# Kernel optimization log

Measured on AMD Instinct MI355X. Metric: run time of the kernel, lower is better.

Reference implementation:

```python
import jax, jax.numpy as jnp
import numpy as np
from jax import lax


def _c1x1(t, w, b=None):
    # t: [B,C,H,W], w: [O,C] (1x1 conv == channel matmul)
    y = jnp.einsum('bchw,oc->bohw', t, w)
    if b is not None:
        y = y + b[None, :, None, None]
    return y


def _mamba(u, in_w, conv_w, conv_b, xproj_w, dt_w, dt_b, A_log, Dp, out_w):
    # u: [B,L,d_model]; Mamba block (mamba_ssm defaults: in/out/x_proj bias=False)
    B, L, _ = u.shape
    d_inner = conv_w.shape[0]
    d_state = A_log.shape[1]
    dt_rank = dt_w.shape[1]
    d_conv = conv_w.shape[2]
    xz = jnp.einsum('bld,ed->ble', u, in_w)          # [B,L,2*d_inner]
    xc, z = xz[..., :d_inner], xz[..., d_inner:]
    # depthwise causal conv1d over seq
    xt = jnp.pad(xc.transpose(0, 2, 1), ((0, 0), (0, 0), (d_conv - 1, 0)))
    xt = lax.conv_general_dilated(xt, conv_w, (1,), 'VALID',
                                  feature_group_count=d_inner,
                                  dimension_numbers=('NCH', 'OIH', 'NCH'))
    xc = jax.nn.silu(xt + conv_b[None, :, None]).transpose(0, 2, 1)  # [B,L,d_inner]
    dbc = jnp.einsum('bld,ed->ble', xc, xproj_w)     # [B,L,dt_rank+2*d_state]
    dt = dbc[..., :dt_rank]
    B_ = dbc[..., dt_rank:dt_rank + d_state]
    C_ = dbc[..., dt_rank + d_state:]
    delta = jax.nn.softplus(jnp.einsum('blr,dr->bld', dt, dt_w) + dt_b)  # [B,L,d_inner]
    A = -jnp.exp(A_log)                              # [d_inner,d_state]
    dA = jnp.exp(delta[..., None] * A)               # [B,L,D,N]
    dBu = delta[..., None] * B_[:, :, None, :] * xc[..., None]
    def step(h, inp):
        dA_t, dBu_t, c_t = inp
        h = dA_t * h + dBu_t                         # [B,D,N]
        y = jnp.einsum('bdn,bn->bd', h, c_t)
        return h, y
    h0 = jnp.zeros((B, d_inner, d_state), dtype=u.dtype)
    _, ys = lax.scan(step, h0, (dA.transpose(1, 0, 2, 3),
                                dBu.transpose(1, 0, 2, 3),
                                C_.transpose(1, 0, 2)))
    y = ys.transpose(1, 0, 2) + xc * Dp              # [B,L,d_inner]
    y = y * jax.nn.silu(z)
    return jnp.einsum('bld,od->blo', y, out_w)       # [B,L,d_model]


def setup_inputs() -> dict:
    key = jax.random.key(0)
    B, C, H, W = 8, 128, 160, 160
    mip, d_in, d_st, d_r, d_cv = 8, 256, 16, 8, 4
    ks = iter(jax.random.split(key, 64))
    def rn(shape, s=0.05):
        return (jax.random.normal(next(ks), shape, dtype=jnp.float32) * s)
    inp = {'x': jax.random.normal(next(ks), (B, C, H, W), dtype=jnp.float32)}
    inp.update(conv1_w=rn((mip, C)), conv1_b=rn((mip,)),
               bn_g=jnp.ones((mip,)), bn_b=jnp.zeros((mip,)),
               bn_m=jnp.zeros((mip,)), bn_v=jnp.ones((mip,)),
               convh_w=rn((C, mip)), convh_b=rn((C,)),
               convw_w=rn((C, mip)), convw_b=rn((C,)),
               mlpx_w1=rn((C, C)), mlpx_b1=rn((C,)), mlpx_w2=rn((C, C)), mlpx_b2=rn((C,)),
               mlpy_w1=rn((C, C)), mlpy_b1=rn((C,)), mlpy_w2=rn((C, C)), mlpy_b2=rn((C,)),
               adjust_w=rn((C, 2 * C)))
    for p in ('mx', 'my'):
        inp[p + '_in_w'] = rn((2 * d_in, C))
        inp[p + '_conv_w'] = rn((d_in, 1, d_cv), 0.3)
        inp[p + '_conv_b'] = rn((d_in,))
        inp[p + '_xproj_w'] = rn((d_r + 2 * d_st, d_in))
        inp[p + '_dt_w'] = rn((d_in, d_r))
        inp[p + '_dt_b'] = rn((d_in,))
        inp[p + '_Alog'] = jnp.log(jnp.broadcast_to(jnp.arange(1, d_st + 1, dtype=jnp.float32), (d_in, d_st)))
        inp[p + '_D'] = jnp.ones((d_in,))
        inp[p + '_out_w'] = rn((C, d_in))
    return inp


def reference(x, conv1_w, conv1_b, bn_g, bn_b, bn_m, bn_v, convh_w, convh_b,
              convw_w, convw_b, mlpx_w1, mlpx_b1, mlpx_w2, mlpx_b2,
              mlpy_w1, mlpy_b1, mlpy_w2, mlpy_b2, adjust_w,
              mx_in_w, mx_conv_w, mx_conv_b, mx_xproj_w, mx_dt_w, mx_dt_b,
              mx_Alog, mx_D, mx_out_w,
              my_in_w, my_conv_w, my_conv_b, my_xproj_w, my_dt_w, my_dt_b,
              my_Alog, my_D, my_out_w):
    B, C, H, W = x.shape
    gelu = lambda t: jax.nn.gelu(t, approximate=False)
    # CoordAttWithMLP
    x_h = x.mean(3, keepdims=True)                      # [B,C,H,1]
    x_w = x.mean(2, keepdims=True).transpose(0, 1, 3, 2)  # [B,C,W,1]
    y = jnp.concatenate([x_h, x_w], axis=2)             # [B,C,H+W,1]
    y = _c1x1(y, conv1_w, conv1_b)
    y = (y - bn_m[None, :, None, None]) * jax.lax.rsqrt(bn_v + 1e-5)[None, :, None, None]
    y = y * bn_g[None, :, None, None] + bn_b[None, :, None, None]
    y = gelu(y)
    a_h = _c1x1(y[:, :, :H], convh_w, convh_b)          # [B,C,H,1] (pre-sigmoid)
    a_w = _c1x1(y[:, :, H:].transpose(0, 1, 3, 2), convw_w, convw_b)  # [B,C,1,W]
    # EfficientMambaAttention00
    ux = x.mean(3).transpose(0, 2, 1)                   # [B,H,C]
    x_x = _mamba(ux, mx_in_w, mx_conv_w, mx_conv_b, mx_xproj_w,
                 mx_dt_w, mx_dt_b, mx_Alog, mx_D, mx_out_w)
    x_x = x_x.transpose(0, 2, 1)[..., None]             # [B,C,H,1]
    x_x = jax.nn.sigmoid(x_x + a_h)
    x_x = _c1x1(gelu(_c1x1(x_x, mlpx_w1, mlpx_b1)), mlpx_w2, mlpx_b2)
    uy = x.mean(2).transpose(0, 2, 1)                   # [B,W,C]
    x_y = _mamba(uy, my_in_w, my_conv_w, my_conv_b, my_xproj_w,
                 my_dt_w, my_dt_b, my_Alog, my_D, my_out_w)
    x_y = x_y.transpose(0, 2, 1)[:, :, None, :]         # [B,C,1,W]
    x_y = jax.nn.sigmoid(x_y + a_w)
    x_y = _c1x1(gelu(_c1x1(x_y, mlpy_w1, mlpy_b1)), mlpy_w2, mlpy_b2)
    # combine
    result_h = jax.nn.sigmoid(a_h) * x_y                # [B,C,H,W]
    result_w = jax.nn.sigmoid(a_w) * x_x                # [B,C,H,W]
    out1 = _c1x1(jnp.concatenate([result_h, result_w], axis=1), adjust_w)
    return x * out1
```

## Files before the change

### kernel.cpp

```cpp
#include <hip/hip_runtime.h>
#include <hip/hip_bf16.h>
#include <math.h>


typedef __attribute__((ext_vector_type(8))) short short8;
typedef __attribute__((ext_vector_type(4))) float f32x4;

#define LDS_BARRIER() do { asm volatile("s_waitcnt lgkmcnt(0)" ::: "memory"); \
                           __builtin_amdgcn_s_barrier(); } while(0)

__device__ __forceinline__ float sigm_(float x){ return 1.f/(1.f+__expf(-x)); }
__device__ __forceinline__ float silu_(float x){ return x/(1.f+__expf(-x)); }
__device__ __forceinline__ float gelu_(float x){ return 0.5f*x*(1.f+erff(x*0.7071067811865476f)); }
__device__ __forceinline__ float softplus_(float x){ return (x>20.f)?x:log1pf(__expf(x)); }

__global__ __launch_bounds__(256) void k_means(const float* __restrict__ x,
                                               float* __restrict__ xh, float* __restrict__ xw){
  int bc = blockIdx.x;
  const float* xt = x + (size_t)bc*25600;
  int tid = threadIdx.x, wave = tid>>6, lane = tid&63;
  __shared__ float part[160][41];
  __shared__ float4 colpart[4][40];
  if (lane < 40){
    float csx=0.f, csy=0.f, csz=0.f, csw=0.f;
    #pragma unroll 4
    for (int i=0;i<40;i++){
      int r = wave*40+i;
      float4 v = ((const float4*)(xt + r*160))[lane];
      csx+=v.x; csy+=v.y; csz+=v.z; csw+=v.w;
      part[r][lane] = (v.x+v.y)+(v.z+v.w);
    }
    colpart[wave][lane] = make_float4(csx,csy,csz,csw);
  }
  __syncthreads();
  if (tid < 160){
    float s = 0.f;
    #pragma unroll
    for (int k=0;k<40;k++) s += part[tid][k];
    xh[(size_t)bc*160 + tid] = s*(1.f/160.f);
  }
  if (tid < 40){
    float4 a=colpart[0][tid], b=colpart[1][tid], c=colpart[2][tid], d=colpart[3][tid];
    float4 s = make_float4((a.x+b.x+c.x+d.x)*(1.f/160.f), (a.y+b.y+c.y+d.y)*(1.f/160.f),
                           (a.z+b.z+c.z+d.z)*(1.f/160.f), (a.w+b.w+c.w+d.w)*(1.f/160.f));
    ((float4*)(xw + (size_t)bc*160))[tid] = s;
  }
}

__global__ __launch_bounds__(256) void k_yahw(
                      const float* __restrict__ xh, const float* __restrict__ xw,
                      const float* __restrict__ w1, const float* __restrict__ b1,
                      const float* __restrict__ bg, const float* __restrict__ bb,
                      const float* __restrict__ bm, const float* __restrict__ bv,
                      const float* __restrict__ wh, const float* __restrict__ bh,
                      const float* __restrict__ ww, const float* __restrict__ bw,
                      float* __restrict__ a_h, float* __restrict__ a_w,
                      float* __restrict__ SHT, float* __restrict__ SW,
                      const float* __restrict__ adjw, __hip_bfloat16* __restrict__ adjwb){
  int blk = blockIdx.x;
  int t = threadIdx.x;
  if (blk >= 320){
    int i = (blk-320)*256 + t;
    if (i < 32768) adjwb[i] = __float2bfloat16(adjw[i]);
    return;
  }
  __shared__ float xS[8][128];
  __shared__ float ppart[256];
  __shared__ float yS[8][9];
  int b = blk/40, pt = blk%40;
  int p0 = pt*8;
  bool isH = (pt < 20);
  const float* src = isH ? xh : xw;
  int pp0 = isH ? p0 : (p0-160);
  {
    int c = t>>1, h2 = t&1;
    float4 v = *(const float4*)(src + ((size_t)(b*128+c))*160 + pp0 + h2*4);
    xS[h2*4+0][c]=v.x; xS[h2*4+1][c]=v.y; xS[h2*4+2][c]=v.z; xS[h2*4+3][c]=v.w;
  }
  __syncthreads();
  {
    int p8 = t>>5, m = (t>>2)&7, q = t&3;
    const float* wrow = w1 + m*128 + q*32;
    const float* xrow = &xS[p8][q*32];
    float acc = 0.f;
    #pragma unroll
    for (int k4=0;k4<8;k4++){
      float4 wv = *(const float4*)(wrow + k4*4);
      float4 uv = *(const float4*)(xrow + k4*4);
      acc += wv.x*uv.x + wv.y*uv.y + wv.z*uv.z + wv.w*uv.w;
    }
    ppart[t] = acc;
  }
  __syncthreads();
  if (t < 64){
    int p8 = t>>3, m = t&7;
    float val = b1[m] + ppart[t*4+0] + ppart[t*4+1] + ppart[t*4+2] + ppart[t*4+3];
    val = (val - bm[m]) * rsqrtf(bv[m] + 1e-5f);
    val = val * bg[m] + bb[m];
    yS[p8][m] = gelu_(val);
  }
  __syncthreads();
  {
    int c = t&127, pg = t>>7;
    const float* wrow2 = (isH ? wh : ww) + c*8;
    float wreg[8];
    #pragma unroll
    for (int m=0;m<8;m++) wreg[m] = wrow2[m];
    float bias = (isH ? bh : bw)[c];
    float accp[4];
    #pragma unroll
    for (int j=0;j<4;j++){
      int p = pg*4 + j;
      float a = bias;
      #pragma unroll
      for (int m=0;m<8;m++) a += wreg[m]*yS[p][m];
      accp[j] = a;
    }
    size_t rowo = ((size_t)(b*128+c))*160 + pp0 + pg*4;
    if (isH){
      *(float4*)(a_h + rowo) = make_float4(accp[0],accp[1],accp[2],accp[3]);
      #pragma unroll
      for (int j=0;j<4;j++)
        SHT[((size_t)(b*160 + p0 + pg*4 + j))*128 + c] = sigm_(accp[j]);
    } else {
      *(float4*)(a_w + rowo) = make_float4(accp[0],accp[1],accp[2],accp[3]);
      *(float4*)(SW + rowo) = make_float4(sigm_(accp[0]),sigm_(accp[1]),
                                          sigm_(accp[2]),sigm_(accp[3]));
    }
  }
}

__global__ __launch_bounds__(256) void k_inproj(
                         const float* __restrict__ xh, const float* __restrict__ xw,
                         const float* __restrict__ inw0, const float* __restrict__ inw1,
                         float* __restrict__ xcpre, float* __restrict__ zb){
  __shared__ float uS[8][128];
  int blk = blockIdx.x;
  int g = blk/160, rem = blk%160, b = rem/20, lt = rem%20, lbase = lt*8;
  int t = threadIdx.x;
  const float* src = (g==0)? xh : xw;
  {
    int c = t>>1, lh = t&1;
    float4 v = *(const float4*)(src + ((size_t)(b*128+c))*160 + lbase + lh*4);
    uS[lh*4+0][c]=v.x; uS[lh*4+1][c]=v.y; uS[lh*4+2][c]=v.z; uS[lh*4+3][c]=v.w;
  }
  __syncthreads();
  const float* inw = (g==0)? inw0 : inw1;
  const float* w0p = inw + (size_t)t*128;
  const float* w1p = inw + (size_t)(t+256)*128;
  float acc0[8]={0,0,0,0,0,0,0,0}, acc1[8]={0,0,0,0,0,0,0,0};
  for (int ct=0; ct<16; ct++){
    float4 wa = *(const float4*)(w0p + ct*8);
    float4 wb = *(const float4*)(w0p + ct*8 + 4);
    float4 wc = *(const float4*)(w1p + ct*8);
    float4 wd = *(const float4*)(w1p + ct*8 + 4);
    #pragma unroll
    for (int l=0;l<8;l++){
      float4 ua = *(const float4*)&uS[l][ct*8];
      float4 ub = *(const float4*)&uS[l][ct*8+4];
      acc0[l] += wa.x*ua.x + wa.y*ua.y + wa.z*ua.z + wa.w*ua.w
               + wb.x*ub.x + wb.y*ub.y + wb.z*ub.z + wb.w*ub.w;
      acc1[l] += wc.x*ua.x + wc.y*ua.y + wc.z*ua.z + wc.w*ua.w
               + wd.x*ub.x + wd.y*ub.y + wd.z*ub.z + wd.w*ub.w;
    }
  }
  size_t ob = ((size_t)(g*8+b)*160 + lbase)*256;
  #pragma unroll
  for (int l=0;l<8;l++){
    xcpre[ob + (size_t)l*256 + t] = acc0[l];
    zb   [ob + (size_t)l*256 + t] = acc1[l];
  }
}

__global__ void k_conv(const float* __restrict__ xcpre,
                       const float* __restrict__ cw0, const float* __restrict__ cb0,
                       const float* __restrict__ cw1, const float* __restrict__ cb1,
                       float* __restrict__ xcb){
  int gid = blockIdx.x*blockDim.x + threadIdx.x;
  if (gid >= 2*8*160*256) return;
  int d = gid & 255; int t = gid >> 8; int l = t % 160; int gb = t / 160; int g = gb >> 3;
  const float* cw = ((g==0)? cw0 : cw1) + d*4;
  float acc = ((g==0)? cb0 : cb1)[d];
  const float* base = xcpre + (size_t)gb*160*256 + d;
  #pragma unroll
  for (int k=0;k<4;k++){
    int ls = l-3+k;
    if (ls>=0) acc += cw[k] * base[(size_t)ls*256];
  }
  xcb[gid] = silu_(acc);
}

__global__ __launch_bounds__(256) void k_xproj(
                        const float* __restrict__ xcb,
                        const float* __restrict__ xp0, const float* __restrict__ xp1,
                        float* __restrict__ dbc){
  __shared__ float xv[16][260];
  int blk = blockIdx.x;
  int g = blk/80, rem = blk%80, b = rem/10, lt = rem%10, lbase = lt*16;
  int t = threadIdx.x;
  size_t base = ((size_t)(g*8+b)*160 + lbase)*256;
  for (int i=t; i<4096; i+=256){ int l=i>>8, d=i&255; xv[l][d] = xcb[base+i]; }
  __syncthreads();
  int l = t>>4, s = t&15;
  const float* xp = (g==0)? xp0 : xp1;
  size_t orow = ((size_t)(g*8+b)*160 + lbase + l)*40;
  for (int q=0;q<3;q++){
    int j = s + q*16;
    if (j >= 40) break;
    const float* w = xp + j*256;
    float acc=0.f;
    for (int dd=0; dd<256; dd+=8){
      float4 wa = *(const float4*)(w+dd);
      float4 wb = *(const float4*)(w+dd+4);
      float4 ua = *(const float4*)&xv[l][dd];
      float4 ub = *(const float4*)&xv[l][dd+4];
      acc += wa.x*ua.x + wa.y*ua.y + wa.z*ua.z + wa.w*ua.w
           + wb.x*ub.x + wb.y*ub.y + wb.z*ub.z + wb.w*ub.w;
    }
    dbc[orow + j] = acc;
  }
}

__global__ __launch_bounds__(256) void k_scan(
                       const float* __restrict__ dbc,
                       const float* __restrict__ xcb, const float* __restrict__ zb,
                       const float* __restrict__ dtw0, const float* __restrict__ dtb0,
                       const float* __restrict__ dtw1, const float* __restrict__ dtb1,
                       const float* __restrict__ Alog0, const float* __restrict__ Alog1,
                       const float* __restrict__ D0, const float* __restrict__ D1,
                       float* __restrict__ ysb){
  __shared__ float dsS[160][16];
  __shared__ float BS [160][16];
  __shared__ float CS [160][16];
  __shared__ float xcS[160][16];
  __shared__ float yS [160][16];
  int blk = blockIdx.x;
  int gb = blk >> 4, dblk = blk & 15, g = gb >> 3;
  int dbase = dblk*16;
  int t = threadIdx.x;
  size_t base = (size_t)gb*160*256;
  const float* db = dbc + (size_t)gb*6400;
  const float* dtwG = (g==0)? dtw0 : dtw1;
  const float* dtbG = (g==0)? dtb0 : dtb1;

  #pragma unroll
  for (int i=0;i<10;i++){
    int item = t + 256*i;
    int l = item>>4, c = item&15;
    const float* r = db + l*40;
    int d = dbase + c;
    const float* wt = dtwG + d*8;
    float4 w0 = *(const float4*)wt;
    float4 w1 = *(const float4*)(wt+4);
    float4 r0 = *(const float4*)r;
    float4 r1 = *(const float4*)(r+4);
    float dt = dtbG[d] + w0.x*r0.x+w0.y*r0.y+w0.z*r0.z+w0.w*r0.w
                       + w1.x*r1.x+w1.y*r1.y+w1.z*r1.z+w1.w*r1.w;
    dsS[l][c] = softplus_(dt);
    BS [l][c] = r[8+c];
    CS [l][c] = r[24+c];
    xcS[l][c] = xcb[base + (size_t)l*256 + dbase + c];
  }
  __syncthreads();

  int dloc = t>>4, n = t&15;
  int d = dbase + dloc;
  float A  = -__expf(((g==0)? Alog0 : Alog1)[d*16+n]);
  float Dd = ((g==0)? D0 : D1)[d];
  float h = 0.f;
  for (int lc=0; lc<160; lc+=8){
    float ds8[8], B8[8], C8[8], xc8[8];
    #pragma unroll
    for (int j=0;j<8;j++){
      ds8[j]=dsS[lc+j][dloc]; B8[j]=BS[lc+j][n];
      C8[j]=CS[lc+j][n];      xc8[j]=xcS[lc+j][dloc];
    }
    #pragma unroll
    for (int j=0;j<8;j++){
      float dA = __expf(ds8[j]*A);
      h = dA*h + ds8[j]*B8[j]*xc8[j];
      float p = h*C8[j];
      p += __shfl_xor(p,1,16); p += __shfl_xor(p,2,16);
      p += __shfl_xor(p,4,16); p += __shfl_xor(p,8,16);
      if (n==0) yS[lc+j][dloc] = p + xc8[j]*Dd;
    }
  }
  __syncthreads();

  #pragma unroll
  for (int i=0;i<10;i++){
    int item = t + 256*i;
    int l = item>>4, c = item&15;
    size_t gi = base + (size_t)l*256 + dbase + c;
    ysb[gi] = yS[l][c] * silu_(zb[gi]);
  }
}

__global__ __launch_bounds__(256) void k_post(
                       const float* __restrict__ ysb,
                       const float* __restrict__ ow0, const float* __restrict__ ow1,
                       const float* __restrict__ a_h, const float* __restrict__ a_w,
                       const float* __restrict__ w1x, const float* __restrict__ b1x,
                       const float* __restrict__ w1y, const float* __restrict__ b1y,
                       const float* __restrict__ w2x, const float* __restrict__ b2x,
                       const float* __restrict__ w2y, const float* __restrict__ b2y,
                       float* __restrict__ QxT, float* __restrict__ Qy){
  __shared__ float ysS[10][256];
  __shared__ float Sc[10][128];
  __shared__ float Sp[10][128];
  int blk = blockIdx.x;
  int g = blk>>7, rem = blk&127, b = rem>>4, lt = rem&15, lbase = lt*10;
  int t = threadIdx.x; int c = t&127, kh = t>>7;
  size_t ybase = ((size_t)(g*8+b)*160 + lbase)*256;
  for (int i=t; i<2560; i+=256) ((float*)ysS)[i] = ysb[ybase+i];
  __syncthreads();
  float acc[10];
  {
    const float* w = ((g==0)? ow0 : ow1) + (size_t)c*256 + kh*128;
    #pragma unroll
    for (int l=0;l<10;l++) acc[l]=0.f;
    for (int ct=0; ct<16; ct++){
      float4 wa = *(const float4*)(w + ct*8);
      float4 wb = *(const float4*)(w + ct*8 + 4);
      #pragma unroll
      for (int l=0;l<10;l++){
        float4 ua = *(const float4*)&ysS[l][kh*128+ct*8];
        float4 ub = *(const float4*)&ysS[l][kh*128+ct*8+4];
        acc[l] += wa.x*ua.x + wa.y*ua.y + wa.z*ua.z + wa.w*ua.w
                + wb.x*ub.x + wb.y*ub.y + wb.z*ub.z + wb.w*ub.w;
      }
    }
  }
  if (kh==1){ for (int l=0;l<10;l++) Sc[l][c] = acc[l]; }
  __syncthreads();
  if (kh==0){
    const float* a = ((g==0)? a_h : a_w) + ((size_t)(b*128+c))*160 + lbase;
    #pragma unroll
    for (int l=0;l<10;l++) Sp[l][c] = sigm_(acc[l] + Sc[l][c] + a[l]);
  }
  __syncthreads();
  {
    const float* w = ((g==0)? w1x : w1y) + (size_t)c*128 + kh*64;
    #pragma unroll
    for (int l=0;l<10;l++) acc[l]=0.f;
    for (int ct=0; ct<8; ct++){
      float4 wa = *(const float4*)(w + ct*8);
      float4 wb = *(const float4*)(w + ct*8 + 4);
      #pragma unroll
      for (int l=0;l<10;l++){
        float4 ua = *(const float4*)&Sp[l][kh*64+ct*8];
        float4 ub = *(const float4*)&Sp[l][kh*64+ct*8+4];
        acc[l] += wa.x*ua.x + wa.y*ua.y + wa.z*ua.z + wa.w*ua.w
                + wb.x*ub.x + wb.y*ub.y + wb.z*ub.z + wb.w*ub.w;
      }
    }
  }
  if (kh==1){ for (int l=0;l<10;l++) Sc[l][c] = acc[l]; }
  __syncthreads();
  if (kh==0){
    float bb = ((g==0)? b1x : b1y)[c];
    float tv[10];
    #pragma unroll
    for (int l=0;l<10;l++) tv[l] = gelu_(bb + acc[l] + Sc[l][c]);
    __syncthreads();
    #pragma unroll
    for (int l=0;l<10;l++) Sp[l][c] = tv[l];
  } else {
    __syncthreads();
  }
  __syncthreads();
  {
    const float* w = ((g==0)? w2x : w2y) + (size_t)c*128 + kh*64;
    #pragma unroll
    for (int l=0;l<10;l++) acc[l]=0.f;
    for (int ct=0; ct<8; ct++){
      float4 wa = *(const float4*)(w + ct*8);
      float4 wb = *(const float4*)(w + ct*8 + 4);
      #pragma unroll
      for (int l=0;l<10;l++){
        float4 ua = *(const float4*)&Sp[l][kh*64+ct*8];
        float4 ub = *(const float4*)&Sp[l][kh*64+ct*8+4];
        acc[l] += wa.x*ua.x + wa.y*ua.y + wa.z*ua.z + wa.w*ua.w
                + wb.x*ub.x + wb.y*ub.y + wb.z*ub.z + wb.w*ub.w;
      }
    }
  }
  if (kh==1){ for (int l=0;l<10;l++) Sc[l][c] = acc[l]; }
  __syncthreads();
  if (kh==0){
    float bb = ((g==0)? b2x : b2y)[c];
    if (g==0){
      #pragma unroll
      for (int l=0;l<10;l++)
        QxT[((size_t)(b*160 + lbase + l))*128 + c] = bb + acc[l] + Sc[l][c];
    } else {
      size_t orow = ((size_t)(b*128+c))*160 + lbase;
      #pragma unroll
      for (int l=0;l<10;l++) Qy[orow + l] = bb + acc[l] + Sc[l][c];
    }
  }
}

__device__ __forceinline__ void build_F(__hip_bfloat16* Fb, float s, const float4* v,
                                        int wg, int kq){
  #pragma unroll
  for (int u=0;u<4;u++){
    int wr = wg*16 + u*4;
    Fb[(wr+0)*136 + kq] = __float2bfloat16(s*v[u].x);
    Fb[(wr+1)*136 + kq] = __float2bfloat16(s*v[u].y);
    Fb[(wr+2)*136 + kq] = __float2bfloat16(s*v[u].z);
    Fb[(wr+3)*136 + kq] = __float2bfloat16(s*v[u].w);
  }
}

__global__ __launch_bounds__(256,4) void k_final_mfma(
                       const float* __restrict__ x,
                       const float* __restrict__ SHT, const float* __restrict__ SW,
                       const float* __restrict__ QxT, const float* __restrict__ Qy,
                       const __hip_bfloat16* __restrict__ adjwb, float* __restrict__ out){
  __shared__ __hip_bfloat16 F[2][32*136];
  int blk0 = blockIdx.x;
  int b = blk0 & 7, inner = blk0 >> 3;
  int ht = inner/5, wq = inner%5;
  int h0 = ht*5;
  int wbase = wq*32;
  int tid = threadIdx.x;
  int kq = tid & 127, wg = tid >> 7;
  int wid = tid>>6, lane = tid&63, quad = lane>>4, l16 = lane&15;

  float s0[5], s1[5];
  #pragma unroll
  for (int j=0;j<5;j++){
    s0[j] = SHT[((size_t)(b*160+h0+j))*128 + kq];
    s1[j] = QxT[((size_t)(b*160+h0+j))*128 + kq];
  }
  size_t prow = ((size_t)(b*128+kq))*160 + wbase + wg*16;
  const float4* rp0 = (const float4*)(Qy + prow);
  const float4* rp1 = (const float4*)(SW + prow);
  float4 v0[4], v1[4];
  #pragma unroll
  for (int u=0;u<4;u++) v0[u] = rp0[u];
  #pragma unroll
  for (int u=0;u<4;u++) v1[u] = rp1[u];

  build_F(F[0], s0[0], v0, wg, kq);
  LDS_BARRIER();

  size_t rowA = ((size_t)(b*128 + wid*32 + l16))*25600 + wbase + quad*4;
  size_t rowB = rowA + (size_t)16*25600;

  #pragma unroll
  for (int j=0;j<5;j++){
    int h = h0 + j;
    float4 xv[2][2];
    #pragma unroll
    for (int nt=0;nt<2;nt++){
      xv[0][nt] = *(const float4*)(x + rowA + (size_t)h*160 + nt*16);
      xv[1][nt] = *(const float4*)(x + rowB + (size_t)h*160 + nt*16);
    }
    f32x4 acc[2][2];
    #pragma unroll
    for (int i=0;i<2;i++)
      #pragma unroll
      for (int nt=0;nt<2;nt++) acc[i][nt] = (f32x4){0.f,0.f,0.f,0.f};

    {
      short8 bf[2][4];
      #pragma unroll
      for (int i=0;i<2;i++){
        const __hip_bfloat16* bp = adjwb + (size_t)(wid*32 + i*16 + l16)*256 + quad*8;
        #pragma unroll
        for (int kc=0;kc<4;kc++) bf[i][kc] = *(const short8*)(bp + kc*32);
      }
      #pragma unroll
      for (int nt=0; nt<2; nt++){
        const __hip_bfloat16* ap = &F[0][(nt*16 + l16)*136 + quad*8];
        #pragma unroll
        for (int kc=0;kc<4;kc++){
          short8 af = *(const short8*)(ap + kc*32);
          acc[0][nt] = __builtin_amdgcn_mfma_f32_16x16x32_bf16(af, bf[0][kc], acc[0][nt], 0,0,0);
          acc[1][nt] = __builtin_amdgcn_mfma_f32_16x16x32_bf16(af, bf[1][kc], acc[1][nt], 0,0,0);
        }
      }
    }
    build_F(F[1], s1[j], v1, wg, kq);
    LDS_BARRIER();

    {
      short8 bf[2][4];
      #pragma unroll
      for (int i=0;i<2;i++){
        const __hip_bfloat16* bp = adjwb + (size_t)(wid*32 + i*16 + l16)*256 + 128 + quad*8;
        #pragma unroll
        for (int kc=0;kc<4;kc++) bf[i][kc] = *(const short8*)(bp + kc*32);
      }
      #pragma unroll
      for (int nt=0; nt<2; nt++){
        const __hip_bfloat16* ap = &F[1][(nt*16 + l16)*136 + quad*8];
        #pragma unroll
        for (int kc=0;kc<4;kc++){
          short8 af = *(const short8*)(ap + kc*32);
          acc[0][nt] = __builtin_amdgcn_mfma_f32_16x16x32_bf16(af, bf[0][kc], acc[0][nt], 0,0,0);
          acc[1][nt] = __builtin_amdgcn_mfma_f32_16x16x32_bf16(af, bf[1][kc], acc[1][nt], 0,0,0);
        }
      }
    }
    if (j<4) build_F(F[0], s0[j+1], v0, wg, kq);

    #pragma unroll
    for (int i=0;i<2;i++){
      size_t rb = (i? rowB : rowA) + (size_t)h*160;
      #pragma unroll
      for (int nt=0; nt<2; nt++){
        f32x4 a = acc[i][nt];
        float4 xvv = xv[i][nt];
        float4 ov = make_float4(xvv.x*a[0], xvv.y*a[1], xvv.z*a[2], xvv.w*a[3]);
        *(float4*)(out + rb + nt*16) = ov;
      }
    }
    LDS_BARRIER();
  }
}

extern "C" void kernel_launch(void* const* d_in, const int* in_sizes, int n_in,
                              void* d_out, int out_size, void* d_ws, size_t ws_size,
                              hipStream_t stream) {
  #define W(i) ((const float*)d_in[i])
  const float* X = W(0);
  float* ws = (float*)d_ws;
  float* xh    = ws;
  float* xw    = xh    + 163840;
  float* ybuf  = xw    + 163840;
  float* ah    = ybuf  + 20480;
  float* aw    = ah    + 163840;
  float* xcpre = aw    + 163840;
  float* zb    = xcpre + 655360;
  float* xcb   = zb    + 655360;
  float* dbc   = xcb   + 655360;
  float* ysb   = dbc   + 102400;
  float* QxT   = ysb   + 655360;
  float* Qy    = QxT   + 163840;
  __hip_bfloat16* adjwb = (__hip_bfloat16*)xcpre;
  float* SHT   = xcpre + 16384;
  float* SW    = SHT   + 163840;

  k_means  <<<1024, 256, 0, stream>>>(X, xh, xw);
  k_inproj <<<320,  256, 0, stream>>>(xh, xw, W(20), W(29), xcpre, zb);
  k_conv   <<<2560, 256, 0, stream>>>(xcpre, W(21), W(22), W(30), W(31), xcb);
  k_yahw   <<<448,  256, 0, stream>>>(xh, xw, W(1), W(2), W(3), W(4), W(5), W(6),
                                      W(7), W(8), W(9), W(10), ah, aw, SHT, SW,
                                      W(19), adjwb);
  k_xproj  <<<160,  256, 0, stream>>>(xcb, W(23), W(32), dbc);
  k_scan   <<<256,  256, 0, stream>>>(dbc, xcb, zb, W(24), W(25), W(33), W(34),
                                      W(26), W(35), W(27), W(36), ysb);
  k_post   <<<256,  256, 0, stream>>>(ysb, W(28), W(37), ah, aw,
                                      W(11), W(12), W(15), W(16),
                                      W(13), W(14), W(17), W(18), QxT, Qy);
  k_final_mfma<<<1280, 256, 0, stream>>>(X, SHT, SW, QxT, Qy, adjwb, (float*)d_out);
  #undef W
}
```

Measured before the change: 423.4 us.

## Merge yahw into xproj launch, rework means reduction, halve post tile

The k_yahw and k_xproj kernels are merged into a single launch that dispatches on block index, which removes one kernel launch and lets the two small workloads share the GPU. k_means now reads coalesced float4 chunks across the whole block and reduces columns with LDS atomics instead of per-wave partial sums. k_post handles 5 sequence positions per block instead of 10 and launches twice as many blocks, trading weight reuse for more parallelism. The LDS atomics could contend, and the merged kernel's footprint is sized by its largest branch.

```diff
diff --git a/kernel.cpp b/kernel.cpp
--- a/kernel.cpp
+++ b/kernel.cpp
@@ -17,116 +17,39 @@
 __global__ __launch_bounds__(256) void k_means(const float* __restrict__ x,
                                                float* __restrict__ xh, float* __restrict__ xw){
   int bc = blockIdx.x;
-  const float* xt = x + (size_t)bc*25600;
-  int tid = threadIdx.x, wave = tid>>6, lane = tid&63;
-  __shared__ float part[160][41];
-  __shared__ float4 colpart[4][40];
-  if (lane < 40){
-    float csx=0.f, csy=0.f, csz=0.f, csw=0.f;
-    #pragma unroll 4
-    for (int i=0;i<40;i++){
-      int r = wave*40+i;
-      float4 v = ((const float4*)(xt + r*160))[lane];
-      csx+=v.x; csy+=v.y; csz+=v.z; csw+=v.w;
-      part[r][lane] = (v.x+v.y)+(v.z+v.w);
-    }
-    colpart[wave][lane] = make_float4(csx,csy,csz,csw);
-  }
-  __syncthreads();
-  if (tid < 160){
+  const float4* xt4 = (const float4*)(x + (size_t)bc*25600);
+  int t = threadIdx.x;
+  __shared__ float hsS[6400];
+  __shared__ float colacc[160];
+  if (t < 160) colacc[t] = 0.f;
+  __syncthreads();
+  #pragma unroll
+  for (int ch=0; ch<5; ch++){
+    float4 vv[5];
+    #pragma unroll
+    for (int j=0;j<5;j++) vv[j] = xt4[(ch*5+j)*256 + t];
+    #pragma unroll
+    for (int j=0;j<5;j++){
+      int idx = (ch*5+j)*256 + t;
+      hsS[idx] = (vv[j].x+vv[j].y)+(vv[j].z+vv[j].w);
+      int col = (idx % 40)*4;
+      atomicAdd(&colacc[col+0], vv[j].x);
+      atomicAdd(&colacc[col+1], vv[j].y);
+      atomicAdd(&colacc[col+2], vv[j].z);
+      atomicAdd(&colacc[col+3], vv[j].w);
+    }
+  }
+  __syncthreads();
+  if (t < 160){
+    const float4* hr4 = (const float4*)&hsS[t*40];
     float s = 0.f;
     #pragma unroll
-    for (int k=0;k<40;k++) s += part[tid][k];
-    xh[(size_t)bc*160 + tid] = s*(1.f/160.f);
-  }
-  if (tid < 40){
-    float4 a=colpart[0][tid], b=colpart[1][tid], c=colpart[2][tid], d=colpart[3][tid];
-    float4 s = make_float4((a.x+b.x+c.x+d.x)*(1.f/160.f), (a.y+b.y+c.y+d.y)*(1.f/160.f),
-                           (a.z+b.z+c.z+d.z)*(1.f/160.f), (a.w+b.w+c.w+d.w)*(1.f/160.f));
-    ((float4*)(xw + (size_t)bc*160))[tid] = s;
-  }
-}
-
-__global__ __launch_bounds__(256) void k_yahw(
-                      const float* __restrict__ xh, const float* __restrict__ xw,
-                      const float* __restrict__ w1, const float* __restrict__ b1,
-                      const float* __restrict__ bg, const float* __restrict__ bb,
-                      const float* __restrict__ bm, const float* __restrict__ bv,
-                      const float* __restrict__ wh, const float* __restrict__ bh,
-                      const float* __restrict__ ww, const float* __restrict__ bw,
-                      float* __restrict__ a_h, float* __restrict__ a_w,
-                      float* __restrict__ SHT, float* __restrict__ SW,
-                      const float* __restrict__ adjw, __hip_bfloat16* __restrict__ adjwb){
-  int blk = blockIdx.x;
-  int t = threadIdx.x;
-  if (blk >= 320){
-    int i = (blk-320)*256 + t;
-    if (i < 32768) adjwb[i] = __float2bfloat16(adjw[i]);
-    return;
-  }
-  __shared__ float xS[8][128];
-  __shared__ float ppart[256];
-  __shared__ float yS[8][9];
-  int b = blk/40, pt = blk%40;
-  int p0 = pt*8;
-  bool isH = (pt < 20);
-  const float* src = isH ? xh : xw;
-  int pp0 = isH ? p0 : (p0-160);
-  {
-    int c = t>>1, h2 = t&1;
-    float4 v = *(const float4*)(src + ((size_t)(b*128+c))*160 + pp0 + h2*4);
-    xS[h2*4+0][c]=v.x; xS[h2*4+1][c]=v.y; xS[h2*4+2][c]=v.z; xS[h2*4+3][c]=v.w;
-  }
-  __syncthreads();
-  {
-    int p8 = t>>5, m = (t>>2)&7, q = t&3;
-    const float* wrow = w1 + m*128 + q*32;
-    const float* xrow = &xS[p8][q*32];
-    float acc = 0.f;
-    #pragma unroll
-    for (int k4=0;k4<8;k4++){
-      float4 wv = *(const float4*)(wrow + k4*4);
-      float4 uv = *(const float4*)(xrow + k4*4);
-      acc += wv.x*uv.x + wv.y*uv.y + wv.z*uv.z + wv.w*uv.w;
-    }
-    ppart[t] = acc;
-  }
-  __syncthreads();
-  if (t < 64){
-    int p8 = t>>3, m = t&7;
-    float val = b1[m] + ppart[t*4+0] + ppart[t*4+1] + ppart[t*4+2] + ppart[t*4+3];
-    val = (val - bm[m]) * rsqrtf(bv[m] + 1e-5f);
-    val = val * bg[m] + bb[m];
-    yS[p8][m] = gelu_(val);
-  }
-  __syncthreads();
-  {
-    int c = t&127, pg = t>>7;
-    const float* wrow2 = (isH ? wh : ww) + c*8;
-    float wreg[8];
-    #pragma unroll
-    for (int m=0;m<8;m++) wreg[m] = wrow2[m];
-    float bias = (isH ? bh : bw)[c];
-    float accp[4];
-    #pragma unroll
-    for (int j=0;j<4;j++){
-      int p = pg*4 + j;
-      float a = bias;
-      #pragma unroll
-      for (int m=0;m<8;m++) a += wreg[m]*yS[p][m];
-      accp[j] = a;
-    }
-    size_t rowo = ((size_t)(b*128+c))*160 + pp0 + pg*4;
-    if (isH){
-      *(float4*)(a_h + rowo) = make_float4(accp[0],accp[1],accp[2],accp[3]);
-      #pragma unroll
-      for (int j=0;j<4;j++)
-        SHT[((size_t)(b*160 + p0 + pg*4 + j))*128 + c] = sigm_(accp[j]);
-    } else {
-      *(float4*)(a_w + rowo) = make_float4(accp[0],accp[1],accp[2],accp[3]);
-      *(float4*)(SW + rowo) = make_float4(sigm_(accp[0]),sigm_(accp[1]),
-                                          sigm_(accp[2]),sigm_(accp[3]));
-    }
+    for (int k=0;k<10;k++){
+      float4 h4 = hr4[k];
+      s += (h4.x+h4.y)+(h4.z+h4.w);
+    }
+    xh[(size_t)bc*160 + t] = s*(1.f/160.f);
+    xw[(size_t)bc*160 + t] = colacc[t]*(1.f/160.f);
   }
 }
 
@@ -190,34 +113,116 @@
   xcb[gid] = silu_(acc);
 }
 
-__global__ __launch_bounds__(256) void k_xproj(
+__global__ __launch_bounds__(256) void k_yx(
                         const float* __restrict__ xcb,
                         const float* __restrict__ xp0, const float* __restrict__ xp1,
-                        float* __restrict__ dbc){
+                        float* __restrict__ dbc,
+                        const float* __restrict__ xh, const float* __restrict__ xw,
+                        const float* __restrict__ w1, const float* __restrict__ b1,
+                        const float* __restrict__ bg, const float* __restrict__ bb,
+                        const float* __restrict__ bm, const float* __restrict__ bv,
+                        const float* __restrict__ wh, const float* __restrict__ bh,
+                        const float* __restrict__ ww, const float* __restrict__ bw,
+                        float* __restrict__ a_h, float* __restrict__ a_w,
+                        float* __restrict__ SHT, float* __restrict__ SW,
+                        const float* __restrict__ adjw, __hip_bfloat16* __restrict__ adjwb){
   __shared__ float xv[16][260];
+  __shared__ float xS[8][128];
+  __shared__ float ppart[256];
+  __shared__ float yS[8][9];
   int blk = blockIdx.x;
-  int g = blk/80, rem = blk%80, b = rem/10, lt = rem%10, lbase = lt*16;
   int t = threadIdx.x;
-  size_t base = ((size_t)(g*8+b)*160 + lbase)*256;
-  for (int i=t; i<4096; i+=256){ int l=i>>8, d=i&255; xv[l][d] = xcb[base+i]; }
-  __syncthreads();
-  int l = t>>4, s = t&15;
-  const float* xp = (g==0)? xp0 : xp1;
-  size_t orow = ((size_t)(g*8+b)*160 + lbase + l)*40;
-  for (int q=0;q<3;q++){
-    int j = s + q*16;
-    if (j >= 40) break;
-    const float* w = xp + j*256;
-    float acc=0.f;
-    for (int dd=0; dd<256; dd+=8){
-      float4 wa = *(const float4*)(w+dd);
-      float4 wb = *(const float4*)(w+dd+4);
-      float4 ua = *(const float4*)&xv[l][dd];
-      float4 ub = *(const float4*)&xv[l][dd+4];
-      acc += wa.x*ua.x + wa.y*ua.y + wa.z*ua.z + wa.w*ua.w
-           + wb.x*ub.x + wb.y*ub.y + wb.z*ub.z + wb.w*ub.w;
-    }
-    dbc[orow + j] = acc;
+  if (blk >= 480){
+    int i = (blk-480)*256 + t;
+    if (i < 32768) adjwb[i] = __float2bfloat16(adjw[i]);
+    return;
+  }
+  if (blk < 160){
+    int g = blk/80, rem = blk%80, b = rem/10, lt = rem%10, lbase = lt*16;
+    size_t base = ((size_t)(g*8+b)*160 + lbase)*256;
+    for (int i=t; i<4096; i+=256){ int l=i>>8, d=i&255; xv[l][d] = xcb[base+i]; }
+    __syncthreads();
+    int l = t>>4, s = t&15;
+    const float* xp = (g==0)? xp0 : xp1;
+    size_t orow = ((size_t)(g*8+b)*160 + lbase + l)*40;
+    for (int q=0;q<3;q++){
+      int j = s + q*16;
+      if (j >= 40) break;
+      const float* w = xp + j*256;
+      float acc=0.f;
+      for (int dd=0; dd<256; dd+=8){
+        float4 wa = *(const float4*)(w+dd);
+        float4 wb = *(const float4*)(w+dd+4);
+        float4 ua = *(const float4*)&xv[l][dd];
+        float4 ub = *(const float4*)&xv[l][dd+4];
+        acc += wa.x*ua.x + wa.y*ua.y + wa.z*ua.z + wa.w*ua.w
+             + wb.x*ub.x + wb.y*ub.y + wb.z*ub.z + wb.w*ub.w;
+      }
+      dbc[orow + j] = acc;
+    }
+    return;
+  }
+  int blk2 = blk - 160;
+  int b = blk2/40, pt = blk2%40;
+  int p0 = pt*8;
+  bool isH = (pt < 20);
+  const float* src = isH ? xh : xw;
+  int pp0 = isH ? p0 : (p0-160);
+  {
+    int c = t>>1, h2 = t&1;
+    float4 v = *(const float4*)(src + ((size_t)(b*128+c))*160 + pp0 + h2*4);
+    xS[h2*4+0][c]=v.x; xS[h2*4+1][c]=v.y; xS[h2*4+2][c]=v.z; xS[h2*4+3][c]=v.w;
+  }
+  __syncthreads();
+  {
+    int p8 = t>>5, m = (t>>2)&7, q = t&3;
+    const float* wrow = w1 + m*128 + q*32;
+    const float* xrow = &xS[p8][q*32];
+    float acc = 0.f;
+    #pragma unroll
+    for (int k4=0;k4<8;k4++){
+      float4 wv = *(const float4*)(wrow + k4*4);
+      float4 uv = *(const float4*)(xrow + k4*4);
+      acc += wv.x*uv.x + wv.y*uv.y + wv.z*uv.z + wv.w*uv.w;
+    }
+    ppart[t] = acc;
+  }
+  __syncthreads();
+  if (t < 64){
+    int p8 = t>>3, m = t&7;
+    float val = b1[m] + ppart[t*4+0] + ppart[t*4+1] + ppart[t*4+2] + ppart[t*4+3];
+    val = (val - bm[m]) * rsqrtf(bv[m] + 1e-5f);
+    val = val * bg[m] + bb[m];
+    yS[p8][m] = gelu_(val);
+  }
+  __syncthreads();
+  {
+    int c = t&127, pg = t>>7;
+    const float* wrow2 = (isH ? wh : ww) + c*8;
+    float wreg[8];
+    #pragma unroll
+    for (int m=0;m<8;m++) wreg[m] = wrow2[m];
+    float bias = (isH ? bh : bw)[c];
+    float accp[4];
+    #pragma unroll
+    for (int j=0;j<4;j++){
+      int p = pg*4 + j;
+      float a = bias;
+      #pragma unroll
+      for (int m=0;m<8;m++) a += wreg[m]*yS[p][m];
+      accp[j] = a;
+    }
+    size_t rowo = ((size_t)(b*128+c))*160 + pp0 + pg*4;
+    if (isH){
+      *(float4*)(a_h + rowo) = make_float4(accp[0],accp[1],accp[2],accp[3]);
+      #pragma unroll
+      for (int j=0;j<4;j++)
+        SHT[((size_t)(b*160 + p0 + pg*4 + j))*128 + c] = sigm_(accp[j]);
+    } else {
+      *(float4*)(a_w + rowo) = make_float4(accp[0],accp[1],accp[2],accp[3]);
+      *(float4*)(SW + rowo) = make_float4(sigm_(accp[0]),sigm_(accp[1]),
+                                          sigm_(accp[2]),sigm_(accp[3]));
+    }
   }
 }
 
@@ -305,25 +310,25 @@
                        const float* __restrict__ w2x, const float* __restrict__ b2x,
                        const float* __restrict__ w2y, const float* __restrict__ b2y,
                        float* __restrict__ QxT, float* __restrict__ Qy){
-  __shared__ float ysS[10][256];
-  __shared__ float Sc[10][128];
-  __shared__ float Sp[10][128];
+  __shared__ float ysS[5][256];
+  __shared__ float Sc[5][128];
+  __shared__ float Sp[5][128];
   int blk = blockIdx.x;
-  int g = blk>>7, rem = blk&127, b = rem>>4, lt = rem&15, lbase = lt*10;
+  int g = blk>>8, rem = blk&255, b = rem>>5, lt = rem&31, lbase = lt*5;
   int t = threadIdx.x; int c = t&127, kh = t>>7;
   size_t ybase = ((size_t)(g*8+b)*160 + lbase)*256;
-  for (int i=t; i<2560; i+=256) ((float*)ysS)[i] = ysb[ybase+i];
-  __syncthreads();
-  float acc[10];
+  for (int i=t; i<1280; i+=256) ((float*)ysS)[i] = ysb[ybase+i];
+  __syncthreads();
+  float acc[5];
   {
     const float* w = ((g==0)? ow0 : ow1) + (size_t)c*256 + kh*128;
     #pragma unroll
-    for (int l=0;l<10;l++) acc[l]=0.f;
+    for (int l=0;l<5;l++) acc[l]=0.f;
     for (int ct=0; ct<16; ct++){
       float4 wa = *(const float4*)(w + ct*8);
       float4 wb = *(const float4*)(w + ct*8 + 4);
       #pragma unroll
-      for (int l=0;l<10;l++){
+      for (int l=0;l<5;l++){
         float4 ua = *(const float4*)&ysS[l][kh*128+ct*8];
         float4 ub = *(const float4*)&ysS[l][kh*128+ct*8+4];
         acc[l] += wa.x*ua.x + wa.y*ua.y + wa.z*ua.z + wa.w*ua.w
@@ -331,23 +336,23 @@
       }
     }
   }
-  if (kh==1){ for (int l=0;l<10;l++) Sc[l][c] = acc[l]; }
+  if (kh==1){ for (int l=0;l<5;l++) Sc[l][c] = acc[l]; }
   __syncthreads();
   if (kh==0){
     const float* a = ((g==0)? a_h : a_w) + ((size_t)(b*128+c))*160 + lbase;
     #pragma unroll
-    for (int l=0;l<10;l++) Sp[l][c] = sigm_(acc[l] + Sc[l][c] + a[l]);
+    for (int l=0;l<5;l++) Sp[l][c] = sigm_(acc[l] + Sc[l][c] + a[l]);
   }
   __syncthreads();
   {
     const float* w = ((g==0)? w1x : w1y) + (size_t)c*128 + kh*64;
     #pragma unroll
-    for (int l=0;l<10;l++) acc[l]=0.f;
+    for (int l=0;l<5;l++) acc[l]=0.f;
     for (int ct=0; ct<8; ct++){
       float4 wa = *(const float4*)(w + ct*8);
       float4 wb = *(const float4*)(w + ct*8 + 4);
       #pragma unroll
-      for (int l=0;l<10;l++){
+      for (int l=0;l<5;l++){
         float4 ua = *(const float4*)&Sp[l][kh*64+ct*8];
         float4 ub = *(const float4*)&Sp[l][kh*64+ct*8+4];
         acc[l] += wa.x*ua.x + wa.y*ua.y + wa.z*ua.z + wa.w*ua.w
@@ -355,16 +360,16 @@
       }
     }
   }
-  if (kh==1){ for (int l=0;l<10;l++) Sc[l][c] = acc[l]; }
+  if (kh==1){ for (int l=0;l<5;l++) Sc[l][c] = acc[l]; }
   __syncthreads();
   if (kh==0){
     float bb = ((g==0)? b1x : b1y)[c];
-    float tv[10];
-    #pragma unroll
-    for (int l=0;l<10;l++) tv[l] = gelu_(bb + acc[l] + Sc[l][c]);
+    float tv[5];
+    #pragma unroll
+    for (int l=0;l<5;l++) tv[l] = gelu_(bb + acc[l] + Sc[l][c]);
     __syncthreads();
     #pragma unroll
-    for (int l=0;l<10;l++) Sp[l][c] = tv[l];
+    for (int l=0;l<5;l++) Sp[l][c] = tv[l];
   } else {
     __syncthreads();
   }
@@ -372,12 +377,12 @@
   {
     const float* w = ((g==0)? w2x : w2y) + (size_t)c*128 + kh*64;
     #pragma unroll
-    for (int l=0;l<10;l++) acc[l]=0.f;
+    for (int l=0;l<5;l++) acc[l]=0.f;
     for (int ct=0; ct<8; ct++){
       float4 wa = *(const float4*)(w + ct*8);
       float4 wb = *(const float4*)(w + ct*8 + 4);
       #pragma unroll
-      for (int l=0;l<10;l++){
+      for (int l=0;l<5;l++){
         float4 ua = *(const float4*)&Sp[l][kh*64+ct*8];
         float4 ub = *(const float4*)&Sp[l][kh*64+ct*8+4];
         acc[l] += wa.x*ua.x + wa.y*ua.y + wa.z*ua.z + wa.w*ua.w
@@ -385,18 +390,18 @@
       }
     }
   }
-  if (kh==1){ for (int l=0;l<10;l++) Sc[l][c] = acc[l]; }
+  if (kh==1){ for (int l=0;l<5;l++) Sc[l][c] = acc[l]; }
   __syncthreads();
   if (kh==0){
     float bb = ((g==0)? b2x : b2y)[c];
     if (g==0){
       #pragma unroll
-      for (int l=0;l<10;l++)
+      for (int l=0;l<5;l++)
         QxT[((size_t)(b*160 + lbase + l))*128 + c] = bb + acc[l] + Sc[l][c];
     } else {
       size_t orow = ((size_t)(b*128+c))*160 + lbase;
       #pragma unroll
-      for (int l=0;l<10;l++) Qy[orow + l] = bb + acc[l] + Sc[l][c];
+      for (int l=0;l<5;l++) Qy[orow + l] = bb + acc[l] + Sc[l][c];
     }
   }
 }
@@ -547,13 +552,13 @@
   k_means  <<<1024, 256, 0, stream>>>(X, xh, xw);
   k_inproj <<<320,  256, 0, stream>>>(xh, xw, W(20), W(29), xcpre, zb);
   k_conv   <<<2560, 256, 0, stream>>>(xcpre, W(21), W(22), W(30), W(31), xcb);
-  k_yahw   <<<448,  256, 0, stream>>>(xh, xw, W(1), W(2), W(3), W(4), W(5), W(6),
+  k_yx     <<<608,  256, 0, stream>>>(xcb, W(23), W(32), dbc,
+                                      xh, xw, W(1), W(2), W(3), W(4), W(5), W(6),
                                       W(7), W(8), W(9), W(10), ah, aw, SHT, SW,
                                       W(19), adjwb);
-  k_xproj  <<<160,  256, 0, stream>>>(xcb, W(23), W(32), dbc);
   k_scan   <<<256,  256, 0, stream>>>(dbc, xcb, zb, W(24), W(25), W(33), W(34),
                                       W(26), W(35), W(27), W(36), ysb);
-  k_post   <<<256,  256, 0, stream>>>(ysb, W(28), W(37), ah, aw,
+  k_post   <<<512,  256, 0, stream>>>(ysb, W(28), W(37), ah, aw,
                                       W(11), W(12), W(15), W(16),
                                       W(13), W(14), W(17), W(18), QxT, Qy);
   k_final_mfma<<<1280, 256, 0, stream>>>(X, SHT, SW, QxT, Qy, adjwb, (float*)d_out);
```

Result: slower. 514.5 us (+21.5%).
